# Kernel tuning notes

Measured on AMD Instinct MI355X. Metric: run time of the kernel, lower is better.

Reference implementation:

```python
import jax, jax.numpy as jnp
import numpy as np

NF, NH, NC, B = 8, 200, 8, 131072  # nFeatures, nHidden, nCls, batch
NEQ = 2

def _lin_init(k, fan_in, fan_out):
    k1, k2 = jax.random.split(k)
    s = 1.0 / np.sqrt(fan_in)
    W = jax.random.uniform(k1, (fan_out, fan_in), minval=-s, maxval=s, dtype=jnp.float32)
    b = jax.random.uniform(k2, (fan_out,), minval=-s, maxval=s, dtype=jnp.float32)
    return W, b

def setup_inputs() -> dict:
    key = jax.random.key(0)
    ks = jax.random.split(key, 6)
    W0, b0 = _lin_init(ks[0], NF, NF)
    W1, b1 = _lin_init(ks[1], NF, NH)
    W2, b2 = _lin_init(ks[2], NH, NH)
    W3, b3 = _lin_init(ks[3], NH, NH)
    W4, b4 = _lin_init(ks[4], NH, NC)
    Q = jnp.eye(NF, dtype=jnp.float32)  # Parameter initialized to identity
    x = jax.random.normal(ks[5], (B, NF), dtype=jnp.float32)
    return dict(x=x, Q=Q, W0=W0, b0=b0, W1=W1, b1=b1, W2=W2, b2=b2, W3=W3, b3=b3, W4=W4, b4=b4)

def _qp_equality(Q, p, A, bvec):
    # min 1/2 z'Qz + p'z  s.t.  A z = b.  (G=0, h=0 => inequality constraints vacuous.)
    # KKT: [Q A'; A 0] [z; nu] = [-p; b], solved batched (tiny 10x10 systems).
    Bn, m, n = A.shape
    Qb = jnp.broadcast_to(Q, (Bn, n, n))
    K = jnp.concatenate([
        jnp.concatenate([Qb, jnp.swapaxes(A, 1, 2)], axis=2),        # [B, n, n+m]
        jnp.concatenate([A, jnp.zeros((Bn, m, m), Q.dtype)], axis=2) # [B, m, n+m]
    ], axis=1)                                                        # [B, n+m, n+m]
    rhs = jnp.concatenate([-p, bvec], axis=1)                         # [B, n+m]
    sol = jnp.linalg.solve(K, rhs[..., None])[..., 0]
    return sol[:, :n]

def reference(x, Q, W0, b0, W1, b1, W2, b2, W3, b3, W4, b4):
    h = x @ W0.T + b0                      # fc0, [B, 8]
    p = -h
    z_ = jnp.zeros_like(h[:, 3])
    o_ = jnp.ones_like(h[:, 3])
    # A[i] = [[0,0,0,0,h[i,3],1,0,0], [0,0,0,0,0,0,h[i,3],1]]  (detached in original)
    A = jnp.stack([
        jnp.stack([z_, z_, z_, z_, h[:, 3], o_, z_, z_], axis=1),
        jnp.stack([z_, z_, z_, z_, z_, z_, h[:, 3], o_], axis=1)], axis=1)  # [B, 2, 8]
    A = jax.lax.stop_gradient(A)  # torch.tensor(...) breaks the graph for A
    bvec = jnp.stack([h[:, 3] * h[:, 4] + h[:, 5],
                      h[:, 3] * h[:, 6] + h[:, 7]], axis=1)  # [B, 2]
    z = _qp_equality(Q, p, A, bvec)        # QPFunction solution, [B, 8]
    y = jax.nn.relu(z @ W1.T + b1)
    y = jax.nn.relu(y @ W2.T + b2)
    y = jax.nn.relu(y @ W3.T + b3)
    return y @ W4.T + b4                   # [B, 8]
```

## Files before the change

### kernel.cpp

```cpp
#include <hip/hip_runtime.h>
#include <math.h>

typedef _Float16 f16;
typedef f16 half8 __attribute__((ext_vector_type(8)));
typedef float floatx4 __attribute__((ext_vector_type(4)));

#define NF 8
#define NH 200
#define NC 8
#define M_BLK 256
#define SCR_W 40

#define WS_QI   0
#define WS_B1P  256
#define WS_B2P  1152
#define WS_B3P  2048
#define WS_WP1  3008
#define WS_WP2  16320
#define WS_WP3  109504
#define WS_WP4  202688
#define WS_NEED 209856

__device__ __forceinline__ void pack_frag(const float* __restrict__ W, int Nv, int Kv,
                                          int nkt, int nks, f16* __restrict__ dst, int gid)
{
    if (gid < nks * nkt * 64) {
        const int ks    = gid / (nkt * 64);
        const int rem   = gid - ks * nkt * 64;
        const int nt    = rem >> 6;
        const int lane  = rem & 63;
        const int n     = nt * 16 + (lane & 15);
        const int kbase = ks * 32 + ((lane >> 4) * 8);
        f16 tmp[8];
#pragma unroll
        for (int j = 0; j < 8; ++j) {
            const int k = kbase + j;
            tmp[j] = (n < Nv && k < Kv) ? (f16)W[n * Kv + k] : (f16)0.0f;
        }
        *(half8*)&dst[(size_t)gid * 8] = *(const half8*)tmp;
    }
}

__global__ void prep_kernel(const float* __restrict__ Q,
                            const float* __restrict__ W1, const float* __restrict__ b1,
                            const float* __restrict__ W2, const float* __restrict__ b2,
                            const float* __restrict__ W3, const float* __restrict__ b3,
                            const float* __restrict__ W4,
                            char* __restrict__ ws)
{
    const int gid = blockIdx.x * 256 + threadIdx.x;
    pack_frag(W1, NH, NF, 13, 1, (f16*)(ws + WS_WP1), gid);
    pack_frag(W2, NH, NH, 13, 7, (f16*)(ws + WS_WP2), gid);
    pack_frag(W3, NH, NH, 13, 7, (f16*)(ws + WS_WP3), gid);
    pack_frag(W4, NC, NH, 1,  7, (f16*)(ws + WS_WP4), gid);
    if (gid < 224) {
        ((float*)(ws + WS_B1P))[gid] = (gid < NH) ? b1[gid] : 0.0f;
        ((float*)(ws + WS_B2P))[gid] = (gid < NH) ? b2[gid] : 0.0f;
        ((float*)(ws + WS_B3P))[gid] = (gid < NH) ? b3[gid] : 0.0f;
    }

    if (blockIdx.x == 0) {
        __shared__ float aug[8][16];
        __shared__ int piv;
        float* Qi = (float*)(ws + WS_QI);
        const int t  = threadIdx.x;
        const bool a = t < 128;
        const int r  = (t >> 4) & 7;
        const int c2 = t & 15;
        if (a) aug[r][c2] = (c2 < 8) ? Q[r * 8 + c2] : ((c2 - 8 == r) ? 1.0f : 0.0f);
        __syncthreads();
        for (int c = 0; c < 8; ++c) {
            if (t == 0) {
                int p = c; float best = fabsf(aug[c][c]);
                for (int rr = c + 1; rr < 8; ++rr) {
                    float v = fabsf(aug[rr][c]);
                    if (v > best) { best = v; p = rr; }
                }
                piv = p;
            }
            __syncthreads();
            const int p = piv;
            float myv = a ? aug[r][c2] : 0.0f;
            __syncthreads();
            if (a) {
                if (r == c)      aug[p][c2] = myv;
                else if (r == p) aug[c][c2] = myv;
            }
            __syncthreads();
            const float pv = aug[c][c];
            __syncthreads();
            if (a && r == c) aug[r][c2] = aug[r][c2] / pv;
            __syncthreads();
            const float fac  = (a && r != c) ? aug[r][c] : 0.0f;
            const float prow = aug[c][c2];
            __syncthreads();
            if (a) aug[r][c2] -= fac * prow;
            __syncthreads();
        }
        if (a && c2 >= 8) Qi[r * 8 + (c2 - 8)] = aug[r][c2];
    }
}

template<int NKS>
__device__ __forceinline__ void layer_slab(const f16* __restrict__ Wp,
                                           const float* __restrict__ biasP,
                                           const half8 (&aIn)[4][7], half8 (&aOut)[4][7],
                                           f16* scr, const int lane,
                                           const int col16, const int g4)
{
#pragma unroll
    for (int p = 0; p < 7; ++p) {
        const int NT = (p < 6) ? 2 : 1;
        const float bv0 = biasP[(2 * p) * 16 + col16];
        const float bv1 = (NT == 2) ? biasP[(2 * p + 1) * 16 + col16] : 0.0f;
        floatx4 acc[4][2];
#pragma unroll
        for (int mt = 0; mt < 4; ++mt) {
            floatx4 v0; v0[0] = bv0; v0[1] = bv0; v0[2] = bv0; v0[3] = bv0;
            acc[mt][0] = v0;
            floatx4 v1; v1[0] = bv1; v1[1] = bv1; v1[2] = bv1; v1[3] = bv1;
            acc[mt][1] = v1;
        }
#pragma unroll
        for (int ks = 0; ks < NKS; ++ks) {
            const half8 bf0 = *(const half8*)&Wp[((size_t)(ks * 13 + 2 * p) * 64 + lane) * 8];
            half8 bf1;
            if (NT == 2) bf1 = *(const half8*)&Wp[((size_t)(ks * 13 + 2 * p + 1) * 64 + lane) * 8];
#pragma unroll
            for (int mt = 0; mt < 4; ++mt) {
                acc[mt][0] = __builtin_amdgcn_mfma_f32_16x16x32_f16(aIn[mt][ks], bf0, acc[mt][0], 0, 0, 0);
                if (NT == 2)
                    acc[mt][1] = __builtin_amdgcn_mfma_f32_16x16x32_f16(aIn[mt][ks], bf1, acc[mt][1], 0, 0, 0);
            }
        }
#pragma unroll
        for (int mt = 0; mt < 4; ++mt) {
#pragma unroll
            for (int r = 0; r < 4; ++r) {
                const int row = mt * 16 + g4 * 4 + r;
                scr[row * SCR_W + col16]      = (f16)fmaxf(acc[mt][0][r], 0.0f);
                if (NT == 2)
                    scr[row * SCR_W + 16 + col16] = (f16)fmaxf(acc[mt][1][r], 0.0f);
                else
                    scr[row * SCR_W + 16 + col16] = (f16)0.0f;
            }
        }
#pragma unroll
        for (int mt = 0; mt < 4; ++mt)
            aOut[mt][p] = *(const half8*)&scr[(mt * 16 + col16) * SCR_W + g4 * 8];
    }
}

__global__ __launch_bounds__(256, 1)
void mlp_slab(const float* __restrict__ x,
              const float* __restrict__ W0, const float* __restrict__ b0,
              const float* __restrict__ b4,
              const char* __restrict__ ws,
              float* __restrict__ out, int B)
{
    __shared__ f16 scrAll[4][64 * SCR_W];
    const int tid   = threadIdx.x;
    const int lane  = tid & 63;
    const int w     = __builtin_amdgcn_readfirstlane(tid >> 6);
    const int col16 = lane & 15;
    const int g4    = lane >> 4;
    f16* scr = &scrAll[w][0];

    const float* Qi  = (const float*)(ws + WS_QI);
    const float* b1p = (const float*)(ws + WS_B1P);
    const float* b2p = (const float*)(ws + WS_B2P);
    const float* b3p = (const float*)(ws + WS_B3P);
    const f16*  Wp1  = (const f16*)(ws + WS_WP1);
    const f16*  Wp2  = (const f16*)(ws + WS_WP2);
    const f16*  Wp3  = (const f16*)(ws + WS_WP3);
    const f16*  Wp4  = (const f16*)(ws + WS_WP4);

    const long g0 = (long)blockIdx.x * M_BLK + w * 64 + lane;
    float xr[NF];
    if (g0 < B) {
        const float4* xp = (const float4*)(x + g0 * NF);
        const float4 A = xp[0], Bv = xp[1];
        xr[0] = A.x; xr[1] = A.y; xr[2] = A.z; xr[3] = A.w;
        xr[4] = Bv.x; xr[5] = Bv.y; xr[6] = Bv.z; xr[7] = Bv.w;
    } else {
#pragma unroll
        for (int i = 0; i < NF; ++i) xr[i] = 0.0f;
    }
    float h[NF];
#pragma unroll
    for (int j = 0; j < NF; ++j) {
        float acc = b0[j];
#pragma unroll
        for (int k = 0; k < NF; ++k) acc = fmaf(W0[j * NF + k], xr[k], acc);
        h[j] = acc;
    }
    float tq[NF], u0[NF], u1[NF];
    const float h3 = h[3];
#pragma unroll
    for (int i = 0; i < NF; ++i) {
        float s = 0.0f;
#pragma unroll
        for (int k = 0; k < NF; ++k) s = fmaf(Qi[i * NF + k], h[k], s);
        tq[i] = s;
        u0[i] = fmaf(Qi[i * NF + 4], h3, Qi[i * NF + 5]);
        u1[i] = fmaf(Qi[i * NF + 6], h3, Qi[i * NF + 7]);
    }
    const float m00 = fmaf(h3, u0[4], u0[5]);
    const float m01 = fmaf(h3, u1[4], u1[5]);
    const float m10 = fmaf(h3, u0[6], u0[7]);
    const float m11 = fmaf(h3, u1[6], u1[7]);
    const float r0  = fmaf(h3, tq[4], tq[5]) - fmaf(h3, h[4], h[5]);
    const float r1  = fmaf(h3, tq[6], tq[7]) - fmaf(h3, h[6], h[7]);
    const float idet = 1.0f / (m00 * m11 - m01 * m10);
    const float nu0 = (m11 * r0 - m01 * r1) * idet;
    const float nu1 = (m00 * r1 - m10 * r0) * idet;

    {
        half8 zh, zz = {};
#pragma unroll
        for (int k = 0; k < 8; ++k) zh[k] = (f16)(tq[k] - u0[k] * nu0 - u1[k] * nu1);
        *(half8*)&scr[lane * SCR_W + 0]  = zh;
        *(half8*)&scr[lane * SCR_W + 8]  = zz;
        *(half8*)&scr[lane * SCR_W + 16] = zz;
        *(half8*)&scr[lane * SCR_W + 24] = zz;
    }

    half8 aA[4][7], aB[4][7];
#pragma unroll
    for (int mt = 0; mt < 4; ++mt)
        aA[mt][0] = *(const half8*)&scr[(mt * 16 + col16) * SCR_W + g4 * 8];

    layer_slab<1>(Wp1, b1p, aA, aB, scr, lane, col16, g4);
    layer_slab<7>(Wp2, b2p, aB, aA, scr, lane, col16, g4);
    layer_slab<7>(Wp3, b3p, aA, aB, scr, lane, col16, g4);

    {
        const float bias4 = b4[col16 & 7];
        floatx4 acc4[4];
#pragma unroll
        for (int mt = 0; mt < 4; ++mt) { floatx4 z_ = {}; acc4[mt] = z_; }
#pragma unroll
        for (int ks = 0; ks < 7; ++ks) {
            const half8 bf = *(const half8*)&Wp4[((size_t)ks * 64 + lane) * 8];
#pragma unroll
            for (int mt = 0; mt < 4; ++mt)
                acc4[mt] = __builtin_amdgcn_mfma_f32_16x16x32_f16(aB[mt][ks], bf, acc4[mt], 0, 0, 0);
        }
        const long rowbase = (long)blockIdx.x * M_BLK + w * 64;
#pragma unroll
        for (int mt = 0; mt < 4; ++mt) {
#pragma unroll
            for (int r = 0; r < 4; ++r) {
                const long g = rowbase + mt * 16 + g4 * 4 + r;
                if (col16 < NC && g < B) out[g * NC + col16] = acc4[mt][r] + bias4;
            }
        }
    }
}

#define BT 64
#define NWAVE 8
#define JB 25
#define CH 8

__device__ __forceinline__ void layer200(const float* __restrict__ in_,
                                         float* __restrict__ out_,
                                         const float* __restrict__ W,
                                         const float* __restrict__ bias,
                                         int j0, int lane)
{
    float acc[JB];
#pragma unroll
    for (int jj = 0; jj < JB; ++jj) acc[jj] = bias[j0 + jj];
#pragma unroll 1
    for (int k0 = 0; k0 < NH; k0 += CH) {
        float a[CH];
#pragma unroll
        for (int u = 0; u < CH; ++u) a[u] = in_[(k0 + u) * BT + lane];
#pragma unroll
        for (int jj = 0; jj < JB; ++jj) {
            const float* wr = W + (j0 + jj) * NH + k0;
#pragma unroll
            for (int u = 0; u < CH; ++u) acc[jj] = fmaf(wr[u], a[u], acc[jj]);
        }
    }
#pragma unroll
    for (int jj = 0; jj < JB; ++jj)
        out_[(j0 + jj) * BT + lane] = fmaxf(acc[jj], 0.0f);
}

__global__ void qinv_kernel(const float* __restrict__ Q, float* __restrict__ Qi)
{
    __shared__ float aug[8][16];
    __shared__ int piv;
    const int t  = threadIdx.x;
    const int r  = t >> 4;
    const int c2 = t & 15;
    aug[r][c2] = (c2 < 8) ? Q[r * 8 + c2] : ((c2 - 8 == r) ? 1.0f : 0.0f);
    __syncthreads();
    for (int c = 0; c < 8; ++c) {
        if (t == 0) {
            int p = c; float best = fabsf(aug[c][c]);
            for (int rr = c + 1; rr < 8; ++rr) {
                float v = fabsf(aug[rr][c]);
                if (v > best) { best = v; p = rr; }
            }
            piv = p;
        }
        __syncthreads();
        const int p = piv;
        float myv = aug[r][c2];
        __syncthreads();
        if (r == c)      aug[p][c2] = myv;
        else if (r == p) aug[c][c2] = myv;
        __syncthreads();
        const float pv = aug[c][c];
        __syncthreads();
        if (r == c) aug[r][c2] = aug[r][c2] / pv;
        __syncthreads();
        const float fac  = (r == c) ? 0.0f : aug[r][c];
        const float prow = aug[c][c2];
        __syncthreads();
        aug[r][c2] -= fac * prow;
        __syncthreads();
    }
    if (c2 >= 8) Qi[r * 8 + (c2 - 8)] = aug[r][c2];
}

__global__ __launch_bounds__(BT * NWAVE, 2)
void mlp_fused(const float* __restrict__ x, const float* __restrict__ Qi,
               const float* __restrict__ W0, const float* __restrict__ b0,
               const float* __restrict__ W1, const float* __restrict__ b1,
               const float* __restrict__ W2, const float* __restrict__ b2,
               const float* __restrict__ W3, const float* __restrict__ b3,
               const float* __restrict__ W4, const float* __restrict__ b4,
               float* __restrict__ out, int B)
{
    __shared__ float actA[NH * BT];
    __shared__ float actB[NH * BT];
    __shared__ float outP[NWAVE * NC * BT];

    const int lane = threadIdx.x & 63;
    const int wid  = __builtin_amdgcn_readfirstlane((int)(threadIdx.x >> 6));
    const int g    = blockIdx.x * BT + lane;
    const int j0   = wid * JB;

    float xr[NF];
    if (g < B) {
        const float4* xp = reinterpret_cast<const float4*>(x + (size_t)g * NF);
        float4 x0 = xp[0], x1 = xp[1];
        xr[0] = x0.x; xr[1] = x0.y; xr[2] = x0.z; xr[3] = x0.w;
        xr[4] = x1.x; xr[5] = x1.y; xr[6] = x1.z; xr[7] = x1.w;
    } else {
#pragma unroll
        for (int i = 0; i < NF; ++i) xr[i] = 0.0f;
    }
    float h[NF];
#pragma unroll
    for (int j = 0; j < NF; ++j) {
        float acc = b0[j];
#pragma unroll
        for (int k = 0; k < NF; ++k) acc = fmaf(W0[j * NF + k], xr[k], acc);
        h[j] = acc;
    }
    float tq[NF], u0[NF], u1[NF];
    const float h3 = h[3];
#pragma unroll
    for (int i = 0; i < NF; ++i) {
        float s = 0.0f;
#pragma unroll
        for (int k = 0; k < NF; ++k) s = fmaf(Qi[i * NF + k], h[k], s);
        tq[i] = s;
        u0[i] = fmaf(Qi[i * NF + 4], h3, Qi[i * NF + 5]);
        u1[i] = fmaf(Qi[i * NF + 6], h3, Qi[i * NF + 7]);
    }
    const float m00 = fmaf(h3, u0[4], u0[5]);
    const float m01 = fmaf(h3, u1[4], u1[5]);
    const float m10 = fmaf(h3, u0[6], u0[7]);
    const float m11 = fmaf(h3, u1[6], u1[7]);
    const float r0  = fmaf(h3, tq[4], tq[5]) - fmaf(h3, h[4], h[5]);
    const float r1  = fmaf(h3, tq[6], tq[7]) - fmaf(h3, h[6], h[7]);
    const float idet = 1.0f / (m00 * m11 - m01 * m10);
    const float nu0 = (m11 * r0 - m01 * r1) * idet;
    const float nu1 = (m00 * r1 - m10 * r0) * idet;
    float z[NF];
#pragma unroll
    for (int i = 0; i < NF; ++i) z[i] = tq[i] - u0[i] * nu0 - u1[i] * nu1;

#pragma unroll
    for (int jj = 0; jj < JB; ++jj) {
        const int j = j0 + jj;
        float acc = b1[j];
#pragma unroll
        for (int k = 0; k < NF; ++k) acc = fmaf(W1[j * NF + k], z[k], acc);
        actA[j * BT + lane] = fmaxf(acc, 0.0f);
    }
    __syncthreads();
    layer200(actA, actB, W2, b2, j0, lane);
    __syncthreads();
    layer200(actB, actA, W3, b3, j0, lane);
    __syncthreads();
    {
        float a[JB];
#pragma unroll
        for (int kk = 0; kk < JB; ++kk) a[kk] = actA[(j0 + kk) * BT + lane];
        float acc[NC];
#pragma unroll
        for (int o = 0; o < NC; ++o) acc[o] = 0.0f;
#pragma unroll
        for (int o = 0; o < NC; ++o) {
            const float* wr = W4 + o * NH + j0;
#pragma unroll
            for (int kk = 0; kk < JB; ++kk) acc[o] = fmaf(wr[kk], a[kk], acc[o]);
        }
#pragma unroll
        for (int o = 0; o < NC; ++o) outP[(wid * NC + o) * BT + lane] = acc[o];
    }
    __syncthreads();
    {
        float s = b4[wid];
#pragma unroll
        for (int w = 0; w < NWAVE; ++w) s += outP[(w * NC + wid) * BT + lane];
        if (g < B) out[(size_t)g * NC + wid] = s;
    }
}

extern "C" void kernel_launch(void* const* d_in, const int* in_sizes, int n_in,
                              void* d_out, int out_size, void* d_ws, size_t ws_size,
                              hipStream_t stream)
{
    const float* x  = (const float*)d_in[0];
    const float* Q  = (const float*)d_in[1];
    const float* W0 = (const float*)d_in[2];
    const float* b0 = (const float*)d_in[3];
    const float* W1 = (const float*)d_in[4];
    const float* b1 = (const float*)d_in[5];
    const float* W2 = (const float*)d_in[6];
    const float* b2 = (const float*)d_in[7];
    const float* W3 = (const float*)d_in[8];
    const float* b3 = (const float*)d_in[9];
    const float* W4 = (const float*)d_in[10];
    const float* b4 = (const float*)d_in[11];
    float* out = (float*)d_out;

    const int B = in_sizes[0] / NF;

    if (ws_size >= WS_NEED) {
        hipLaunchKernelGGL(prep_kernel, dim3(23), dim3(256), 0, stream,
                           Q, W1, b1, W2, b2, W3, b3, W4, (char*)d_ws);
        hipLaunchKernelGGL(mlp_slab, dim3((B + M_BLK - 1) / M_BLK), dim3(256), 0, stream,
                           x, W0, b0, b4, (const char*)d_ws, out, B);
    } else {
        float* Qi = (float*)d_ws;
        hipLaunchKernelGGL(qinv_kernel, dim3(1), dim3(128), 0, stream, Q, Qi);
        hipLaunchKernelGGL(mlp_fused, dim3((B + BT - 1) / BT), dim3(BT * NWAVE), 0, stream,
                           x, Qi, W0, b0, W1, b1, W2, b2, W3, b3, W4, b4, out, B);
    }
}
```

Baseline: 52.74 us.

## Use single-wave 48-row blocks with register-prefetched MFMA weight fragments

Replaces the 4-wave, 256-row block with a single-wave block handling 48 rows (three 16-row M tiles), launched as 64 threads with two blocks per CU. Each layer pass now loads the next weight fragment into registers while the current MFMAs issue, including across pass and layer boundaries, to hide global/L2 load latency. The smaller tile lowers register pressure and gives many more independent waves, at the cost of reloading the weights for every 48 rows instead of every 64. The workspace threshold is raised, which could send smaller workspaces to the slower fallback path.

```diff
diff --git a/kernel.cpp b/kernel.cpp
--- a/kernel.cpp
+++ b/kernel.cpp
@@ -8,8 +8,10 @@
 #define NF 8
 #define NH 200
 #define NC 8
-#define M_BLK 256
-#define SCR_W 40
+#define MT 3
+#define M_BLK 48
+#define SCR_W 36
+#define FRAG 512
 
 #define WS_QI   0
 #define WS_B1P  256
@@ -19,7 +21,7 @@
 #define WS_WP2  16320
 #define WS_WP3  109504
 #define WS_WP4  202688
-#define WS_NEED 209856
+#define WS_NEED 212000
 
 __device__ __forceinline__ void pack_frag(const float* __restrict__ W, int Nv, int Kv,
                                           int nkt, int nks, f16* __restrict__ dst, int gid)
@@ -101,70 +103,90 @@
     }
 }
 
+__device__ __forceinline__ half8 ldfrag(const f16* __restrict__ p, int lane)
+{
+    return *(const half8*)&p[lane * 8];
+}
+
 template<int NKS>
-__device__ __forceinline__ void layer_slab(const f16* __restrict__ Wp,
-                                           const float* __restrict__ biasP,
-                                           const half8 (&aIn)[4][7], half8 (&aOut)[4][7],
-                                           f16* scr, const int lane,
-                                           const int col16, const int g4)
-{
-#pragma unroll
-    for (int p = 0; p < 7; ++p) {
-        const int NT = (p < 6) ? 2 : 1;
-        const float bv0 = biasP[(2 * p) * 16 + col16];
-        const float bv1 = (NT == 2) ? biasP[(2 * p + 1) * 16 + col16] : 0.0f;
-        floatx4 acc[4][2];
-#pragma unroll
-        for (int mt = 0; mt < 4; ++mt) {
-            floatx4 v0; v0[0] = bv0; v0[1] = bv0; v0[2] = bv0; v0[3] = bv0;
-            acc[mt][0] = v0;
-            floatx4 v1; v1[0] = bv1; v1[1] = bv1; v1[2] = bv1; v1[3] = bv1;
-            acc[mt][1] = v1;
+struct Layer {
+    template<int P>
+    static __device__ __forceinline__ void pass(const f16* __restrict__ Wp,
+        const f16* __restrict__ nextLayer, const float* __restrict__ biasP,
+        const half8 (&aIn)[MT][7], half8 (&aOut)[MT][7], f16* __restrict__ scr,
+        half8& bf0, half8& bf1, const int lane, const int col16, const int g4)
+    {
+        constexpr int NT = (P < 6) ? 2 : 1;
+        const f16* nxt = (P < 6) ? (Wp + 2 * (P + 1) * FRAG) : nextLayer;
+
+        const float bv0 = biasP[(2 * P) * 16 + col16];
+        const float bv1 = (NT == 2) ? biasP[(2 * P + 1) * 16 + col16] : 0.0f;
+        floatx4 a0[MT], a1[MT];
+#pragma unroll
+        for (int mt = 0; mt < MT; ++mt) {
+            floatx4 v; v[0] = bv0; v[1] = bv0; v[2] = bv0; v[3] = bv0; a0[mt] = v;
+            floatx4 w; w[0] = bv1; w[1] = bv1; w[2] = bv1; w[3] = bv1; a1[mt] = w;
         }
 #pragma unroll
         for (int ks = 0; ks < NKS; ++ks) {
-            const half8 bf0 = *(const half8*)&Wp[((size_t)(ks * 13 + 2 * p) * 64 + lane) * 8];
-            half8 bf1;
-            if (NT == 2) bf1 = *(const half8*)&Wp[((size_t)(ks * 13 + 2 * p + 1) * 64 + lane) * 8];
-#pragma unroll
-            for (int mt = 0; mt < 4; ++mt) {
-                acc[mt][0] = __builtin_amdgcn_mfma_f32_16x16x32_f16(aIn[mt][ks], bf0, acc[mt][0], 0, 0, 0);
+            half8 n0, n1;
+            if (ks + 1 < NKS) {
+                n0 = ldfrag(Wp + ((ks + 1) * 13 + 2 * P) * FRAG, lane);
+                if (NT == 2) n1 = ldfrag(Wp + ((ks + 1) * 13 + 2 * P + 1) * FRAG, lane);
+                else         n1 = bf1;
+            } else {
+                n0 = ldfrag(nxt, lane);
+                n1 = ldfrag(nxt + FRAG, lane);
+            }
+#pragma unroll
+            for (int mt = 0; mt < MT; ++mt) {
+                a0[mt] = __builtin_amdgcn_mfma_f32_16x16x32_f16(aIn[mt][ks], bf0, a0[mt], 0, 0, 0);
                 if (NT == 2)
-                    acc[mt][1] = __builtin_amdgcn_mfma_f32_16x16x32_f16(aIn[mt][ks], bf1, acc[mt][1], 0, 0, 0);
-            }
-        }
-#pragma unroll
-        for (int mt = 0; mt < 4; ++mt) {
+                    a1[mt] = __builtin_amdgcn_mfma_f32_16x16x32_f16(aIn[mt][ks], bf1, a1[mt], 0, 0, 0);
+            }
+            bf0 = n0; bf1 = n1;
+        }
+#pragma unroll
+        for (int mt = 0; mt < MT; ++mt) {
 #pragma unroll
             for (int r = 0; r < 4; ++r) {
                 const int row = mt * 16 + g4 * 4 + r;
-                scr[row * SCR_W + col16]      = (f16)fmaxf(acc[mt][0][r], 0.0f);
-                if (NT == 2)
-                    scr[row * SCR_W + 16 + col16] = (f16)fmaxf(acc[mt][1][r], 0.0f);
-                else
-                    scr[row * SCR_W + 16 + col16] = (f16)0.0f;
-            }
-        }
-#pragma unroll
-        for (int mt = 0; mt < 4; ++mt)
-            aOut[mt][p] = *(const half8*)&scr[(mt * 16 + col16) * SCR_W + g4 * 8];
-    }
-}
-
-__global__ __launch_bounds__(256, 1)
-void mlp_slab(const float* __restrict__ x,
-              const float* __restrict__ W0, const float* __restrict__ b0,
-              const float* __restrict__ b4,
-              const char* __restrict__ ws,
-              float* __restrict__ out, int B)
-{
-    __shared__ f16 scrAll[4][64 * SCR_W];
-    const int tid   = threadIdx.x;
-    const int lane  = tid & 63;
-    const int w     = __builtin_amdgcn_readfirstlane(tid >> 6);
+                scr[row * SCR_W + col16] = (f16)fmaxf(a0[mt][r], 0.0f);
+                scr[row * SCR_W + 16 + col16] =
+                    (NT == 2) ? (f16)fmaxf(a1[mt][r], 0.0f) : (f16)0.0f;
+            }
+        }
+#pragma unroll
+        for (int mt = 0; mt < MT; ++mt)
+            aOut[mt][P] = *(const half8*)&scr[(mt * 16 + col16) * SCR_W + g4 * 8];
+    }
+
+    static __device__ __forceinline__ void run(const f16* __restrict__ Wp,
+        const f16* __restrict__ nextLayer, const float* __restrict__ biasP,
+        const half8 (&aIn)[MT][7], half8 (&aOut)[MT][7], f16* __restrict__ scr,
+        half8& bf0, half8& bf1, const int lane, const int col16, const int g4)
+    {
+        pass<0>(Wp, nextLayer, biasP, aIn, aOut, scr, bf0, bf1, lane, col16, g4);
+        pass<1>(Wp, nextLayer, biasP, aIn, aOut, scr, bf0, bf1, lane, col16, g4);
+        pass<2>(Wp, nextLayer, biasP, aIn, aOut, scr, bf0, bf1, lane, col16, g4);
+        pass<3>(Wp, nextLayer, biasP, aIn, aOut, scr, bf0, bf1, lane, col16, g4);
+        pass<4>(Wp, nextLayer, biasP, aIn, aOut, scr, bf0, bf1, lane, col16, g4);
+        pass<5>(Wp, nextLayer, biasP, aIn, aOut, scr, bf0, bf1, lane, col16, g4);
+        pass<6>(Wp, nextLayer, biasP, aIn, aOut, scr, bf0, bf1, lane, col16, g4);
+    }
+};
+
+__global__ __launch_bounds__(64, 2)
+void mlp_slab1(const float* __restrict__ x,
+               const float* __restrict__ W0, const float* __restrict__ b0,
+               const float* __restrict__ b4,
+               const char* __restrict__ ws,
+               float* __restrict__ out, int B)
+{
+    __shared__ f16 scr[M_BLK * SCR_W];
+    const int lane  = threadIdx.x & 63;
     const int col16 = lane & 15;
     const int g4    = lane >> 4;
-    f16* scr = &scrAll[w][0];
 
     const float* Qi  = (const float*)(ws + WS_QI);
     const float* b1p = (const float*)(ws + WS_B1P);
@@ -175,9 +197,12 @@
     const f16*  Wp3  = (const f16*)(ws + WS_WP3);
     const f16*  Wp4  = (const f16*)(ws + WS_WP4);
 
-    const long g0 = (long)blockIdx.x * M_BLK + w * 64 + lane;
+    half8 bf0 = ldfrag(Wp1, lane);
+    half8 bf1 = ldfrag(Wp1 + FRAG, lane);
+
+    const long g0 = (long)blockIdx.x * M_BLK + lane;
     float xr[NF];
-    if (g0 < B) {
+    if (lane < M_BLK && g0 < B) {
         const float4* xp = (const float4*)(x + g0 * NF);
         const float4 A = xp[0], Bv = xp[1];
         xr[0] = A.x; xr[1] = A.y; xr[2] = A.z; xr[3] = A.w;
@@ -215,7 +240,7 @@
     const float nu0 = (m11 * r0 - m01 * r1) * idet;
     const float nu1 = (m00 * r1 - m10 * r0) * idet;
 
-    {
+    if (lane < M_BLK) {
         half8 zh, zz = {};
 #pragma unroll
         for (int k = 0; k < 8; ++k) zh[k] = (f16)(tq[k] - u0[k] * nu0 - u1[k] * nu1);
@@ -225,30 +250,31 @@
         *(half8*)&scr[lane * SCR_W + 24] = zz;
     }
 
-    half8 aA[4][7], aB[4][7];
-#pragma unroll
-    for (int mt = 0; mt < 4; ++mt)
+    half8 aA[MT][7], aB[MT][7];
+#pragma unroll
+    for (int mt = 0; mt < MT; ++mt)
         aA[mt][0] = *(const half8*)&scr[(mt * 16 + col16) * SCR_W + g4 * 8];
 
-    layer_slab<1>(Wp1, b1p, aA, aB, scr, lane, col16, g4);
-    layer_slab<7>(Wp2, b2p, aB, aA, scr, lane, col16, g4);
-    layer_slab<7>(Wp3, b3p, aA, aB, scr, lane, col16, g4);
+    Layer<1>::run(Wp1, Wp2, b1p, aA, aB, scr, bf0, bf1, lane, col16, g4);
+    Layer<7>::run(Wp2, Wp3, b2p, aB, aA, scr, bf0, bf1, lane, col16, g4);
+    Layer<7>::run(Wp3, Wp4, b3p, aA, aB, scr, bf0, bf1, lane, col16, g4);
 
     {
+        floatx4 acc4[MT];
+#pragma unroll
+        for (int mt = 0; mt < MT; ++mt) { floatx4 z_ = {}; acc4[mt] = z_; }
+#pragma unroll
+        for (int ks = 0; ks < 7; ++ks) {
+            half8 n0 = (ks < 6) ? ldfrag(Wp4 + (ks + 1) * FRAG, lane) : bf0;
+#pragma unroll
+            for (int mt = 0; mt < MT; ++mt)
+                acc4[mt] = __builtin_amdgcn_mfma_f32_16x16x32_f16(aB[mt][ks], bf0, acc4[mt], 0, 0, 0);
+            bf0 = n0;
+        }
         const float bias4 = b4[col16 & 7];
-        floatx4 acc4[4];
-#pragma unroll
-        for (int mt = 0; mt < 4; ++mt) { floatx4 z_ = {}; acc4[mt] = z_; }
-#pragma unroll
-        for (int ks = 0; ks < 7; ++ks) {
-            const half8 bf = *(const half8*)&Wp4[((size_t)ks * 64 + lane) * 8];
-#pragma unroll
-            for (int mt = 0; mt < 4; ++mt)
-                acc4[mt] = __builtin_amdgcn_mfma_f32_16x16x32_f16(aB[mt][ks], bf, acc4[mt], 0, 0, 0);
-        }
-        const long rowbase = (long)blockIdx.x * M_BLK + w * 64;
-#pragma unroll
-        for (int mt = 0; mt < 4; ++mt) {
+        const long rowbase = (long)blockIdx.x * M_BLK;
+#pragma unroll
+        for (int mt = 0; mt < MT; ++mt) {
 #pragma unroll
             for (int r = 0; r < 4; ++r) {
                 const long g = rowbase + mt * 16 + g4 * 4 + r;
@@ -448,7 +474,7 @@
     if (ws_size >= WS_NEED) {
         hipLaunchKernelGGL(prep_kernel, dim3(23), dim3(256), 0, stream,
                            Q, W1, b1, W2, b2, W3, b3, W4, (char*)d_ws);
-        hipLaunchKernelGGL(mlp_slab, dim3((B + M_BLK - 1) / M_BLK), dim3(256), 0, stream,
+        hipLaunchKernelGGL(mlp_slab1, dim3((B + M_BLK - 1) / M_BLK), dim3(64), 0, stream,
                            x, W0, b0, b4, (const char*)d_ws, out, B);
     } else {
         float* Qi = (float*)d_ws;
```

Measured after the change: 55.43 us. 1.05x slower.

## Use single-wave blocks with register double-buffered weight fragment prefetch across layers

Applied to the files above, without the earlier changes.

Replaces the 4-wave 256-row block with a one-wave 64-row block and restructures each hidden layer so the next column-pair's weight fragments are loaded into a second register buffer while the current pair's MFMAs run, including prefetching the next layer's first fragments. The full 200-wide activation row is now staged in LDS (wider scratch) and reloaded once per layer instead of per column pair, and the bias add moves into the epilogue. This aims to hide global/L2 weight-load latency behind MFMA work, at the cost of much higher register pressure (two 14-fragment buffers plus 28 activation fragments) and more blocks each re-reading all weights.

```diff
diff --git a/kernel.cpp b/kernel.cpp
--- a/kernel.cpp
+++ b/kernel.cpp
@@ -8,8 +8,9 @@
 #define NF 8
 #define NH 200
 #define NC 8
-#define M_BLK 256
-#define SCR_W 40
+#define M_BLK 64
+#define SCR_W 232
+#define FRAG 512
 
 #define WS_QI   0
 #define WS_B1P  256
@@ -19,7 +20,7 @@
 #define WS_WP2  16320
 #define WS_WP3  109504
 #define WS_WP4  202688
-#define WS_NEED 209856
+#define WS_NEED 212000
 
 __device__ __forceinline__ void pack_frag(const float* __restrict__ W, int Nv, int Kv,
                                           int nkt, int nks, f16* __restrict__ dst, int gid)
@@ -101,70 +102,127 @@
     }
 }
 
-template<int NKS>
-__device__ __forceinline__ void layer_slab(const f16* __restrict__ Wp,
-                                           const float* __restrict__ biasP,
-                                           const half8 (&aIn)[4][7], half8 (&aOut)[4][7],
-                                           f16* scr, const int lane,
-                                           const int col16, const int g4)
-{
-#pragma unroll
-    for (int p = 0; p < 7; ++p) {
-        const int NT = (p < 6) ? 2 : 1;
-        const float bv0 = biasP[(2 * p) * 16 + col16];
-        const float bv1 = (NT == 2) ? biasP[(2 * p + 1) * 16 + col16] : 0.0f;
-        floatx4 acc[4][2];
-#pragma unroll
-        for (int mt = 0; mt < 4; ++mt) {
-            floatx4 v0; v0[0] = bv0; v0[1] = bv0; v0[2] = bv0; v0[3] = bv0;
-            acc[mt][0] = v0;
-            floatx4 v1; v1[0] = bv1; v1[1] = bv1; v1[2] = bv1; v1[3] = bv1;
-            acc[mt][1] = v1;
-        }
-#pragma unroll
-        for (int ks = 0; ks < NKS; ++ks) {
-            const half8 bf0 = *(const half8*)&Wp[((size_t)(ks * 13 + 2 * p) * 64 + lane) * 8];
-            half8 bf1;
-            if (NT == 2) bf1 = *(const half8*)&Wp[((size_t)(ks * 13 + 2 * p + 1) * 64 + lane) * 8];
-#pragma unroll
-            for (int mt = 0; mt < 4; ++mt) {
-                acc[mt][0] = __builtin_amdgcn_mfma_f32_16x16x32_f16(aIn[mt][ks], bf0, acc[mt][0], 0, 0, 0);
-                if (NT == 2)
-                    acc[mt][1] = __builtin_amdgcn_mfma_f32_16x16x32_f16(aIn[mt][ks], bf1, acc[mt][1], 0, 0, 0);
-            }
-        }
-#pragma unroll
-        for (int mt = 0; mt < 4; ++mt) {
-#pragma unroll
-            for (int r = 0; r < 4; ++r) {
-                const int row = mt * 16 + g4 * 4 + r;
-                scr[row * SCR_W + col16]      = (f16)fmaxf(acc[mt][0][r], 0.0f);
-                if (NT == 2)
-                    scr[row * SCR_W + 16 + col16] = (f16)fmaxf(acc[mt][1][r], 0.0f);
-                else
-                    scr[row * SCR_W + 16 + col16] = (f16)0.0f;
-            }
-        }
+struct FB { half8 f[7][2]; };
+
+__device__ __forceinline__ half8 ldf(const f16* __restrict__ p, int lane)
+{
+    return *(const half8*)&p[lane * 8];
+}
+
+template<int NKS, int NT, int NKT>
+__device__ __forceinline__ void loadp(const f16* __restrict__ Wp, int pp, FB& w, int lane)
+{
+#pragma unroll
+    for (int ks = 0; ks < NKS; ++ks)
+#pragma unroll
+        for (int t = 0; t < NT; ++t)
+            w.f[ks][t] = ldf(Wp + (size_t)(ks * NKT + 2 * pp + t) * FRAG, lane);
+}
+
+template<int NKS, int NT>
+__device__ __forceinline__ void mma_pass(const half8 (&aIn)[4][7], const FB& w,
+                                         floatx4 (&acc)[4][2])
+{
+#pragma unroll
+    for (int ks = 0; ks < NKS; ++ks)
 #pragma unroll
         for (int mt = 0; mt < 4; ++mt)
-            aOut[mt][p] = *(const half8*)&scr[(mt * 16 + col16) * SCR_W + g4 * 8];
-    }
-}
-
-__global__ __launch_bounds__(256, 1)
-void mlp_slab(const float* __restrict__ x,
-              const float* __restrict__ W0, const float* __restrict__ b0,
-              const float* __restrict__ b4,
-              const char* __restrict__ ws,
-              float* __restrict__ out, int B)
-{
-    __shared__ f16 scrAll[4][64 * SCR_W];
-    const int tid   = threadIdx.x;
-    const int lane  = tid & 63;
-    const int w     = __builtin_amdgcn_readfirstlane(tid >> 6);
+#pragma unroll
+            for (int t = 0; t < NT; ++t)
+                acc[mt][t] = __builtin_amdgcn_mfma_f32_16x16x32_f16(
+                    aIn[mt][ks], w.f[ks][t], acc[mt][t], 0, 0, 0);
+}
+
+template<int NT>
+__device__ __forceinline__ void epil(const floatx4 (&acc)[4][2], float b0, float b1,
+                                     f16* __restrict__ scr, int pp, int col16, int g4)
+{
+#pragma unroll
+    for (int mt = 0; mt < 4; ++mt)
+#pragma unroll
+        for (int r = 0; r < 4; ++r) {
+            const int row = mt * 16 + g4 * 4 + r;
+            scr[row * SCR_W + 2 * pp * 16 + col16] = (f16)fmaxf(acc[mt][0][r] + b0, 0.0f);
+            if (NT == 2)
+                scr[row * SCR_W + (2 * pp + 1) * 16 + col16] = (f16)fmaxf(acc[mt][1][r] + b1, 0.0f);
+        }
+}
+
+template<int LK, int NXK, int NXNT, int NXNKT>
+__device__ __forceinline__ void layer13(const f16* __restrict__ Wp,
+                                        const f16* __restrict__ WpN,
+                                        const float* __restrict__ biasP,
+                                        half8 (&aIn)[4][7], FB& w0, FB& w1,
+                                        f16* __restrict__ scr,
+                                        int lane, int col16, int g4)
+{
+    {
+        loadp<LK, 2, 13>(Wp, 1, w1, lane);
+        const float b0 = biasP[0 * 16 + col16], b1 = biasP[1 * 16 + col16];
+        floatx4 acc[4][2] = {};
+        mma_pass<LK, 2>(aIn, w0, acc);
+        epil<2>(acc, b0, b1, scr, 0, col16, g4);
+    }
+    {
+        loadp<LK, 2, 13>(Wp, 2, w0, lane);
+        const float b0 = biasP[2 * 16 + col16], b1 = biasP[3 * 16 + col16];
+        floatx4 acc[4][2] = {};
+        mma_pass<LK, 2>(aIn, w1, acc);
+        epil<2>(acc, b0, b1, scr, 1, col16, g4);
+    }
+    {
+        loadp<LK, 2, 13>(Wp, 3, w1, lane);
+        const float b0 = biasP[4 * 16 + col16], b1 = biasP[5 * 16 + col16];
+        floatx4 acc[4][2] = {};
+        mma_pass<LK, 2>(aIn, w0, acc);
+        epil<2>(acc, b0, b1, scr, 2, col16, g4);
+    }
+    {
+        loadp<LK, 2, 13>(Wp, 4, w0, lane);
+        const float b0 = biasP[6 * 16 + col16], b1 = biasP[7 * 16 + col16];
+        floatx4 acc[4][2] = {};
+        mma_pass<LK, 2>(aIn, w1, acc);
+        epil<2>(acc, b0, b1, scr, 3, col16, g4);
+    }
+    {
+        loadp<LK, 2, 13>(Wp, 5, w1, lane);
+        const float b0 = biasP[8 * 16 + col16], b1 = biasP[9 * 16 + col16];
+        floatx4 acc[4][2] = {};
+        mma_pass<LK, 2>(aIn, w0, acc);
+        epil<2>(acc, b0, b1, scr, 4, col16, g4);
+    }
+    {
+        loadp<LK, 1, 13>(Wp, 6, w0, lane);
+        const float b0 = biasP[10 * 16 + col16], b1 = biasP[11 * 16 + col16];
+        floatx4 acc[4][2] = {};
+        mma_pass<LK, 2>(aIn, w1, acc);
+        epil<2>(acc, b0, b1, scr, 5, col16, g4);
+    }
+    {
+        loadp<NXK, NXNT, NXNKT>(WpN, 0, w1, lane);
+        const float b0 = biasP[12 * 16 + col16];
+        floatx4 acc[4][2] = {};
+        mma_pass<LK, 1>(aIn, w0, acc);
+        epil<1>(acc, b0, 0.0f, scr, 6, col16, g4);
+    }
+#pragma unroll
+    for (int mt = 0; mt < 4; ++mt)
+#pragma unroll
+        for (int ks = 0; ks < 7; ++ks)
+            aIn[mt][ks] = *(const half8*)&scr[(mt * 16 + col16) * SCR_W + ks * 32 + g4 * 8];
+}
+
+__global__ __launch_bounds__(64, 1)
+void mlp_slab2(const float* __restrict__ x,
+               const float* __restrict__ W0, const float* __restrict__ b0,
+               const float* __restrict__ b4,
+               const char* __restrict__ ws,
+               float* __restrict__ out, int B)
+{
+    __shared__ f16 scr[M_BLK * SCR_W];
+    const int lane  = threadIdx.x & 63;
     const int col16 = lane & 15;
     const int g4    = lane >> 4;
-    f16* scr = &scrAll[w][0];
 
     const float* Qi  = (const float*)(ws + WS_QI);
     const float* b1p = (const float*)(ws + WS_B1P);
@@ -175,7 +233,17 @@
     const f16*  Wp3  = (const f16*)(ws + WS_WP3);
     const f16*  Wp4  = (const f16*)(ws + WS_WP4);
 
-    const long g0 = (long)blockIdx.x * M_BLK + w * 64 + lane;
+    FB wA, wB;
+    loadp<1, 2, 13>(Wp1, 0, wA, lane);
+
+    {
+        half8 zz = {};
+        *(half8*)&scr[lane * SCR_W + 208] = zz;
+        *(half8*)&scr[lane * SCR_W + 216] = zz;
+        *(half8*)&scr[lane * SCR_W + 224] = zz;
+    }
+
+    const long g0 = (long)blockIdx.x * M_BLK + lane;
     float xr[NF];
     if (g0 < B) {
         const float4* xp = (const float4*)(x + g0 * NF);
@@ -225,35 +293,33 @@
         *(half8*)&scr[lane * SCR_W + 24] = zz;
     }
 
-    half8 aA[4][7], aB[4][7];
+    half8 aIn[4][7];
 #pragma unroll
     for (int mt = 0; mt < 4; ++mt)
-        aA[mt][0] = *(const half8*)&scr[(mt * 16 + col16) * SCR_W + g4 * 8];
-
-    layer_slab<1>(Wp1, b1p, aA, aB, scr, lane, col16, g4);
-    layer_slab<7>(Wp2, b2p, aB, aA, scr, lane, col16, g4);
-    layer_slab<7>(Wp3, b3p, aA, aB, scr, lane, col16, g4);
-
-    {
-        const float bias4 = b4[col16 & 7];
-        floatx4 acc4[4];
-#pragma unroll
-        for (int mt = 0; mt < 4; ++mt) { floatx4 z_ = {}; acc4[mt] = z_; }
-#pragma unroll
-        for (int ks = 0; ks < 7; ++ks) {
-            const half8 bf = *(const half8*)&Wp4[((size_t)ks * 64 + lane) * 8];
+        aIn[mt][0] = *(const half8*)&scr[(mt * 16 + col16) * SCR_W + g4 * 8];
+
+    layer13<1, 7, 2, 13>(Wp1, Wp2, b1p, aIn, wA, wB, scr, lane, col16, g4);
+    layer13<7, 7, 2, 13>(Wp2, Wp3, b2p, aIn, wB, wA, scr, lane, col16, g4);
+    layer13<7, 7, 1, 1 >(Wp3, Wp4, b3p, aIn, wA, wB, scr, lane, col16, g4);
+
+    {
+        floatx4 a4[4] = {};
+#pragma unroll
+        for (int ks = 0; ks < 7; ++ks)
 #pragma unroll
             for (int mt = 0; mt < 4; ++mt)
-                acc4[mt] = __builtin_amdgcn_mfma_f32_16x16x32_f16(aB[mt][ks], bf, acc4[mt], 0, 0, 0);
-        }
-        const long rowbase = (long)blockIdx.x * M_BLK + w * 64;
-#pragma unroll
-        for (int mt = 0; mt < 4; ++mt) {
-#pragma unroll
-            for (int r = 0; r < 4; ++r) {
-                const long g = rowbase + mt * 16 + g4 * 4 + r;
-                if (col16 < NC && g < B) out[g * NC + col16] = acc4[mt][r] + bias4;
-            }
+                a4[mt] = __builtin_amdgcn_mfma_f32_16x16x32_f16(
+                    aIn[mt][ks], wB.f[ks][0], a4[mt], 0, 0, 0);
+        if (col16 < NC) {
+            const float bias4 = b4[col16];
+            const long rowbase = (long)blockIdx.x * M_BLK;
+#pragma unroll
+            for (int mt = 0; mt < 4; ++mt)
+#pragma unroll
+                for (int r = 0; r < 4; ++r) {
+                    const long g = rowbase + mt * 16 + g4 * 4 + r;
+                    if (g < B) out[g * NC + col16] = a4[mt][r] + bias4;
+                }
         }
     }
 }
@@ -448,7 +514,7 @@
     if (ws_size >= WS_NEED) {
         hipLaunchKernelGGL(prep_kernel, dim3(23), dim3(256), 0, stream,
                            Q, W1, b1, W2, b2, W3, b3, W4, (char*)d_ws);
-        hipLaunchKernelGGL(mlp_slab, dim3((B + M_BLK - 1) / M_BLK), dim3(256), 0, stream,
+        hipLaunchKernelGGL(mlp_slab2, dim3((B + M_BLK - 1) / M_BLK), dim3(64), 0, stream,
                            x, W0, b0, b4, (const char*)d_ws, out, B);
     } else {
         float* Qi = (float*)d_ws;
```

Measured after the change: 49.92 us. -5.4%, faster.

## Split hidden-layer N tiles across two waves sharing a 64-row block with prefetched weights

Applied to the files above, without the earlier changes.

Replaces the per-wave 64-row slab kernel with a 128-thread block in which two waves share one 64-row tile. Each wave computes about half of the 13 output column tiles per layer and writes full activations to shared LDS, with block barriers between layers. Weight fragments for the next tile or layer are prefetched into registers while the current MFMAs run. This cuts redundant weight loads per row and register pressure, at the cost of more __syncthreads and a larger LDS footprint per block. WS_NEED is raised, which can change which path runs if the workspace is small.

```diff
diff --git a/kernel.cpp b/kernel.cpp
--- a/kernel.cpp
+++ b/kernel.cpp
@@ -8,8 +8,9 @@
 #define NF 8
 #define NH 200
 #define NC 8
-#define M_BLK 256
-#define SCR_W 40
+#define M_BLK 64
+#define SCR_W 232
+#define FRAG 512
 
 #define WS_QI   0
 #define WS_B1P  256
@@ -19,7 +20,7 @@
 #define WS_WP2  16320
 #define WS_WP3  109504
 #define WS_WP4  202688
-#define WS_NEED 209856
+#define WS_NEED 212000
 
 __device__ __forceinline__ void pack_frag(const float* __restrict__ W, int Nv, int Kv,
                                           int nkt, int nks, f16* __restrict__ dst, int gid)
@@ -101,70 +102,84 @@
     }
 }
 
-template<int NKS>
-__device__ __forceinline__ void layer_slab(const f16* __restrict__ Wp,
-                                           const float* __restrict__ biasP,
-                                           const half8 (&aIn)[4][7], half8 (&aOut)[4][7],
-                                           f16* scr, const int lane,
-                                           const int col16, const int g4)
-{
-#pragma unroll
-    for (int p = 0; p < 7; ++p) {
-        const int NT = (p < 6) ? 2 : 1;
-        const float bv0 = biasP[(2 * p) * 16 + col16];
-        const float bv1 = (NT == 2) ? biasP[(2 * p + 1) * 16 + col16] : 0.0f;
-        floatx4 acc[4][2];
-#pragma unroll
-        for (int mt = 0; mt < 4; ++mt) {
-            floatx4 v0; v0[0] = bv0; v0[1] = bv0; v0[2] = bv0; v0[3] = bv0;
-            acc[mt][0] = v0;
-            floatx4 v1; v1[0] = bv1; v1[1] = bv1; v1[2] = bv1; v1[3] = bv1;
-            acc[mt][1] = v1;
-        }
-#pragma unroll
-        for (int ks = 0; ks < NKS; ++ks) {
-            const half8 bf0 = *(const half8*)&Wp[((size_t)(ks * 13 + 2 * p) * 64 + lane) * 8];
-            half8 bf1;
-            if (NT == 2) bf1 = *(const half8*)&Wp[((size_t)(ks * 13 + 2 * p + 1) * 64 + lane) * 8];
-#pragma unroll
-            for (int mt = 0; mt < 4; ++mt) {
-                acc[mt][0] = __builtin_amdgcn_mfma_f32_16x16x32_f16(aIn[mt][ks], bf0, acc[mt][0], 0, 0, 0);
-                if (NT == 2)
-                    acc[mt][1] = __builtin_amdgcn_mfma_f32_16x16x32_f16(aIn[mt][ks], bf1, acc[mt][1], 0, 0, 0);
+__device__ __forceinline__ half8 ldf(const f16* __restrict__ p, int lane)
+{
+    return *(const half8*)&p[lane * 8];
+}
+
+__device__ __forceinline__ void epilT(const floatx4 (&acc)[4], float bv,
+                                      f16* __restrict__ scr, int tile,
+                                      int col16, int g4)
+{
+#pragma unroll
+    for (int mt = 0; mt < 4; ++mt)
+#pragma unroll
+        for (int r = 0; r < 4; ++r)
+            scr[(mt * 16 + g4 * 4 + r) * SCR_W + tile * 16 + col16] =
+                (f16)fmaxf(acc[mt][r] + bv, 0.0f);
+}
+
+template<int LK, int NTILES, int LKN, int NKTN>
+__device__ __forceinline__ void layer_run(
+    const f16* __restrict__ Wp, int tbase,
+    const f16* __restrict__ WpN, int tbaseN,
+    const float* __restrict__ biasP,
+    const half8 (&aIn)[4][7], half8 (&fb)[7],
+    f16* __restrict__ scr, int lane, int col16, int g4)
+{
+#pragma unroll
+    for (int p = 0; p < NTILES; ++p) {
+        const float bv = biasP[(tbase + p) * 16 + col16];
+        const bool last = (p + 1 == NTILES);
+        const f16* nb = last ? (WpN + (size_t)tbaseN * FRAG)
+                             : (Wp + (size_t)(tbase + p + 1) * FRAG);
+        const size_t nstride = (size_t)(last ? NKTN : 13) * FRAG;
+        floatx4 acc[4] = {};
+#pragma unroll
+        for (int ks = 0; ks < LK; ++ks) {
+#pragma unroll
+            for (int mt = 0; mt < 4; ++mt)
+                acc[mt] = __builtin_amdgcn_mfma_f32_16x16x32_f16(
+                    aIn[mt][ks], fb[ks], acc[mt], 0, 0, 0);
+            if (LK == 7)
+                fb[ks] = ldf(nb + ks * nstride, lane);
+        }
+        if (LK != 7) {
+            if (!last) fb[0] = ldf(nb, lane);
+            else {
+#pragma unroll
+                for (int ks = 0; ks < LKN; ++ks)
+                    fb[ks] = ldf(nb + ks * nstride, lane);
             }
         }
-#pragma unroll
-        for (int mt = 0; mt < 4; ++mt) {
-#pragma unroll
-            for (int r = 0; r < 4; ++r) {
-                const int row = mt * 16 + g4 * 4 + r;
-                scr[row * SCR_W + col16]      = (f16)fmaxf(acc[mt][0][r], 0.0f);
-                if (NT == 2)
-                    scr[row * SCR_W + 16 + col16] = (f16)fmaxf(acc[mt][1][r], 0.0f);
-                else
-                    scr[row * SCR_W + 16 + col16] = (f16)0.0f;
-            }
-        }
-#pragma unroll
-        for (int mt = 0; mt < 4; ++mt)
-            aOut[mt][p] = *(const half8*)&scr[(mt * 16 + col16) * SCR_W + g4 * 8];
-    }
-}
-
-__global__ __launch_bounds__(256, 1)
-void mlp_slab(const float* __restrict__ x,
-              const float* __restrict__ W0, const float* __restrict__ b0,
-              const float* __restrict__ b4,
-              const char* __restrict__ ws,
-              float* __restrict__ out, int B)
-{
-    __shared__ f16 scrAll[4][64 * SCR_W];
+        epilT(acc, bv, scr, tbase + p, col16, g4);
+    }
+}
+
+__device__ __forceinline__ void readA(half8 (&aIn)[4][7], const f16* __restrict__ scr,
+                                      int col16, int g4)
+{
+#pragma unroll
+    for (int mt = 0; mt < 4; ++mt)
+#pragma unroll
+        for (int ks = 0; ks < 7; ++ks)
+            aIn[mt][ks] = *(const half8*)&scr[(mt * 16 + col16) * SCR_W + ks * 32 + g4 * 8];
+}
+
+__global__ __launch_bounds__(128, 2)
+void mlp_ns(const float* __restrict__ x,
+            const float* __restrict__ W0, const float* __restrict__ b0,
+            const float* __restrict__ b4,
+            const char* __restrict__ ws,
+            float* __restrict__ out, int B)
+{
+    __shared__ f16 scr[M_BLK * SCR_W];
     const int tid   = threadIdx.x;
     const int lane  = tid & 63;
-    const int w     = __builtin_amdgcn_readfirstlane(tid >> 6);
+    const int wid   = __builtin_amdgcn_readfirstlane(tid >> 6);
     const int col16 = lane & 15;
     const int g4    = lane >> 4;
-    f16* scr = &scrAll[w][0];
+    const int tb    = wid ? 7 : 0;
 
     const float* Qi  = (const float*)(ws + WS_QI);
     const float* b1p = (const float*)(ws + WS_B1P);
@@ -175,85 +190,112 @@
     const f16*  Wp3  = (const f16*)(ws + WS_WP3);
     const f16*  Wp4  = (const f16*)(ws + WS_WP4);
 
-    const long g0 = (long)blockIdx.x * M_BLK + w * 64 + lane;
-    float xr[NF];
-    if (g0 < B) {
-        const float4* xp = (const float4*)(x + g0 * NF);
-        const float4 A = xp[0], Bv = xp[1];
-        xr[0] = A.x; xr[1] = A.y; xr[2] = A.z; xr[3] = A.w;
-        xr[4] = Bv.x; xr[5] = Bv.y; xr[6] = Bv.z; xr[7] = Bv.w;
-    } else {
-#pragma unroll
-        for (int i = 0; i < NF; ++i) xr[i] = 0.0f;
-    }
-    float h[NF];
-#pragma unroll
-    for (int j = 0; j < NF; ++j) {
-        float acc = b0[j];
-#pragma unroll
-        for (int k = 0; k < NF; ++k) acc = fmaf(W0[j * NF + k], xr[k], acc);
-        h[j] = acc;
-    }
-    float tq[NF], u0[NF], u1[NF];
-    const float h3 = h[3];
-#pragma unroll
-    for (int i = 0; i < NF; ++i) {
-        float s = 0.0f;
-#pragma unroll
-        for (int k = 0; k < NF; ++k) s = fmaf(Qi[i * NF + k], h[k], s);
-        tq[i] = s;
-        u0[i] = fmaf(Qi[i * NF + 4], h3, Qi[i * NF + 5]);
-        u1[i] = fmaf(Qi[i * NF + 6], h3, Qi[i * NF + 7]);
-    }
-    const float m00 = fmaf(h3, u0[4], u0[5]);
-    const float m01 = fmaf(h3, u1[4], u1[5]);
-    const float m10 = fmaf(h3, u0[6], u0[7]);
-    const float m11 = fmaf(h3, u1[6], u1[7]);
-    const float r0  = fmaf(h3, tq[4], tq[5]) - fmaf(h3, h[4], h[5]);
-    const float r1  = fmaf(h3, tq[6], tq[7]) - fmaf(h3, h[6], h[7]);
-    const float idet = 1.0f / (m00 * m11 - m01 * m10);
-    const float nu0 = (m11 * r0 - m01 * r1) * idet;
-    const float nu1 = (m00 * r1 - m10 * r0) * idet;
+    half8 fb[7];
+    fb[0] = ldf(Wp1 + (size_t)tb * FRAG, lane);
+
+    if (tid < M_BLK) {
+        half8 zz = {};
+        *(half8*)&scr[tid * SCR_W + 208] = zz;
+        *(half8*)&scr[tid * SCR_W + 216] = zz;
+        *(half8*)&scr[tid * SCR_W + 224] = zz;
+
+        const long g0 = (long)blockIdx.x * M_BLK + tid;
+        float xr[NF];
+        if (g0 < B) {
+            const float4* xp = (const float4*)(x + g0 * NF);
+            const float4 A = xp[0], Bv = xp[1];
+            xr[0] = A.x; xr[1] = A.y; xr[2] = A.z; xr[3] = A.w;
+            xr[4] = Bv.x; xr[5] = Bv.y; xr[6] = Bv.z; xr[7] = Bv.w;
+        } else {
+#pragma unroll
+            for (int i = 0; i < NF; ++i) xr[i] = 0.0f;
+        }
+        float h[NF];
+#pragma unroll
+        for (int j = 0; j < NF; ++j) {
+            float acc = b0[j];
+#pragma unroll
+            for (int k = 0; k < NF; ++k) acc = fmaf(W0[j * NF + k], xr[k], acc);
+            h[j] = acc;
+        }
+        float tq[NF], u0[NF], u1[NF];
+        const float h3 = h[3];
+#pragma unroll
+        for (int i = 0; i < NF; ++i) {
+            float s = 0.0f;
+#pragma unroll
+            for (int k = 0; k < NF; ++k) s = fmaf(Qi[i * NF + k], h[k], s);
+            tq[i] = s;
+            u0[i] = fmaf(Qi[i * NF + 4], h3, Qi[i * NF + 5]);
+            u1[i] = fmaf(Qi[i * NF + 6], h3, Qi[i * NF + 7]);
+        }
+        const float m00 = fmaf(h3, u0[4], u0[5]);
+        const float m01 = fmaf(h3, u1[4], u1[5]);
+        const float m10 = fmaf(h3, u0[6], u0[7]);
+        const float m11 = fmaf(h3, u1[6], u1[7]);
+        const float r0  = fmaf(h3, tq[4], tq[5]) - fmaf(h3, h[4], h[5]);
+        const float r1  = fmaf(h3, tq[6], tq[7]) - fmaf(h3, h[6], h[7]);
+        const float idet = 1.0f / (m00 * m11 - m01 * m10);
+        const float nu0 = (m11 * r0 - m01 * r1) * idet;
+        const float nu1 = (m00 * r1 - m10 * r0) * idet;
+
+        half8 zh, zz2 = {};
+#pragma unroll
+        for (int k = 0; k < 8; ++k) zh[k] = (f16)(tq[k] - u0[k] * nu0 - u1[k] * nu1);
+        *(half8*)&scr[tid * SCR_W + 0]  = zh;
+        *(half8*)&scr[tid * SCR_W + 8]  = zz2;
+        *(half8*)&scr[tid * SCR_W + 16] = zz2;
+        *(half8*)&scr[tid * SCR_W + 24] = zz2;
+    }
+    __syncthreads();
+
+    half8 aIn[4][7];
+#pragma unroll
+    for (int mt = 0; mt < 4; ++mt)
+        aIn[mt][0] = *(const half8*)&scr[(mt * 16 + col16) * SCR_W + g4 * 8];
+    __syncthreads();
+
+    if (wid == 0) layer_run<1, 7, 7, 13>(Wp1, 0, Wp2, 0, b1p, aIn, fb, scr, lane, col16, g4);
+    else          layer_run<1, 6, 7, 13>(Wp1, 7, Wp2, 7, b1p, aIn, fb, scr, lane, col16, g4);
+    __syncthreads();
+    readA(aIn, scr, col16, g4);
+    __syncthreads();
+
+    if (wid == 0) layer_run<7, 7, 7, 13>(Wp2, 0, Wp3, 0, b2p, aIn, fb, scr, lane, col16, g4);
+    else          layer_run<7, 6, 7, 13>(Wp2, 7, Wp3, 7, b2p, aIn, fb, scr, lane, col16, g4);
+    __syncthreads();
+    readA(aIn, scr, col16, g4);
+    __syncthreads();
+
+    if (wid == 0) layer_run<7, 7, 7, 1>(Wp3, 0, Wp4, 0, b3p, aIn, fb, scr, lane, col16, g4);
+    else          layer_run<7, 6, 7, 1>(Wp3, 7, Wp4, 0, b3p, aIn, fb, scr, lane, col16, g4);
+    __syncthreads();
 
     {
-        half8 zh, zz = {};
-#pragma unroll
-        for (int k = 0; k < 8; ++k) zh[k] = (f16)(tq[k] - u0[k] * nu0 - u1[k] * nu1);
-        *(half8*)&scr[lane * SCR_W + 0]  = zh;
-        *(half8*)&scr[lane * SCR_W + 8]  = zz;
-        *(half8*)&scr[lane * SCR_W + 16] = zz;
-        *(half8*)&scr[lane * SCR_W + 24] = zz;
-    }
-
-    half8 aA[4][7], aB[4][7];
-#pragma unroll
-    for (int mt = 0; mt < 4; ++mt)
-        aA[mt][0] = *(const half8*)&scr[(mt * 16 + col16) * SCR_W + g4 * 8];
-
-    layer_slab<1>(Wp1, b1p, aA, aB, scr, lane, col16, g4);
-    layer_slab<7>(Wp2, b2p, aB, aA, scr, lane, col16, g4);
-    layer_slab<7>(Wp3, b3p, aA, aB, scr, lane, col16, g4);
-
-    {
-        const float bias4 = b4[col16 & 7];
-        floatx4 acc4[4];
-#pragma unroll
-        for (int mt = 0; mt < 4; ++mt) { floatx4 z_ = {}; acc4[mt] = z_; }
-#pragma unroll
-        for (int ks = 0; ks < 7; ++ks) {
-            const half8 bf = *(const half8*)&Wp4[((size_t)ks * 64 + lane) * 8];
-#pragma unroll
-            for (int mt = 0; mt < 4; ++mt)
-                acc4[mt] = __builtin_amdgcn_mfma_f32_16x16x32_f16(aB[mt][ks], bf, acc4[mt], 0, 0, 0);
-        }
-        const long rowbase = (long)blockIdx.x * M_BLK + w * 64;
-#pragma unroll
-        for (int mt = 0; mt < 4; ++mt) {
-#pragma unroll
-            for (int r = 0; r < 4; ++r) {
-                const long g = rowbase + mt * 16 + g4 * 4 + r;
-                if (col16 < NC && g < B) out[g * NC + col16] = acc4[mt][r] + bias4;
-            }
+        half8 aw[2][7];
+#pragma unroll
+        for (int m2 = 0; m2 < 2; ++m2)
+#pragma unroll
+            for (int ks = 0; ks < 7; ++ks)
+                aw[m2][ks] = *(const half8*)&scr[((wid * 2 + m2) * 16 + col16) * SCR_W
+                                                 + ks * 32 + g4 * 8];
+        floatx4 a4[2] = {};
+#pragma unroll
+        for (int ks = 0; ks < 7; ++ks)
+#pragma unroll
+            for (int m2 = 0; m2 < 2; ++m2)
+                a4[m2] = __builtin_amdgcn_mfma_f32_16x16x32_f16(
+                    aw[m2][ks], fb[ks], a4[m2], 0, 0, 0);
+        if (col16 < NC) {
+            const float bias4 = b4[col16];
+            const long rowbase = (long)blockIdx.x * M_BLK + wid * 32;
+#pragma unroll
+            for (int m2 = 0; m2 < 2; ++m2)
+#pragma unroll
+                for (int r = 0; r < 4; ++r) {
+                    const long g = rowbase + m2 * 16 + g4 * 4 + r;
+                    if (g < B) out[g * NC + col16] = a4[m2][r] + bias4;
+                }
         }
     }
 }
@@ -448,7 +490,7 @@
     if (ws_size >= WS_NEED) {
         hipLaunchKernelGGL(prep_kernel, dim3(23), dim3(256), 0, stream,
                            Q, W1, b1, W2, b2, W3, b3, W4, (char*)d_ws);
-        hipLaunchKernelGGL(mlp_slab, dim3((B + M_BLK - 1) / M_BLK), dim3(256), 0, stream,
+        hipLaunchKernelGGL(mlp_ns, dim3((B + M_BLK - 1) / M_BLK), dim3(128), 0, stream,
                            x, W0, b0, b4, (const char*)d_ws, out, B);
     } else {
         float* Qi = (float*)d_ws;
```

Result: faster. 48.77 us (-7.5%).
